# Kernel optimization log

Measured on AMD Instinct MI355X. Metric: run time of the kernel, lower is better.

## Reference

```python
import math
import jax, jax.numpy as jnp
import numpy as np

NUM_HEADS = 16
HIDDEN = 1024
FILL = -10000000000000.0


def setup_inputs() -> dict:
    key = jax.random.key(0)
    ks = jax.random.split(key, 12)
    B, S, H = 4, 2048, HIDDEN
    scale = 1.0 / math.sqrt(H)
    inp = {
        "query": jax.random.normal(ks[0], (B, S, H), jnp.float32),
        "key": jax.random.normal(ks[1], (B, S, H), jnp.float32),
        "value": jax.random.normal(ks[2], (B, S, H), jnp.float32),
        "mask": jnp.ones((B, S), jnp.float32),
        # torch.nn.Linear weights are [out, in]; y = x @ W.T + b
        "Wq": jax.random.normal(ks[3], (H, H), jnp.float32) * scale,
        "bq": jax.random.normal(ks[4], (H,), jnp.float32) * 0.01,
        "Wk": jax.random.normal(ks[5], (H, H), jnp.float32) * scale,
        "bk": jax.random.normal(ks[6], (H,), jnp.float32) * 0.01,
        "Wv": jax.random.normal(ks[7], (H, H), jnp.float32) * scale,
        "bv": jax.random.normal(ks[8], (H,), jnp.float32) * 0.01,
        "Wo": jax.random.normal(ks[9], (H, H), jnp.float32) * scale,
        "bo": jax.random.normal(ks[10], (H,), jnp.float32) * 0.01,
    }
    return inp


def reference(query, key, value, mask, Wq, bq, Wk, bk, Wv, bv, Wo, bo):
    B, S, H = query.shape
    nh = NUM_HEADS
    dh = H // nh

    def proj(x, W, b):
        # [B,S,H] -> [B,nh,S,dh]
        y = x @ W.T + b
        return y.reshape(B, S, nh, dh).transpose(0, 2, 1, 3)

    q = proj(query, Wq, bq)
    k = proj(key, Wk, bk)
    v = proj(value, Wv, bv)

    # mask_tril=True: combined padding + causal mask [B,1,S,S]
    tril = jnp.tril(jnp.ones((S, S), query.dtype))
    m = jnp.einsum("bs,ls->bls", mask, tril)[:, None]

    scores = jnp.einsum("bhqd,bhkd->bhqk", q, k) / math.sqrt(dh)
    scores = jnp.where(m == 0, jnp.asarray(FILL, scores.dtype), scores)
    probs = jax.nn.softmax(scores, axis=-1)  # dropout p=0 -> identity

    out = jnp.einsum("bhqv,bhvd->bhqd", probs, v)
    out = out.transpose(0, 2, 1, 3).reshape(B, S, H)
    return out @ Wo.T + bo
```

## Files before the change

kernel.cpp:

```cpp
#include <hip/hip_runtime.h>
#include <hip/hip_bf16.h>
#include <math.h>

#define BATCH 4
#define SEQ   2048
#define HID   1024
#define NH    16
#define DH    64
#define MTOT  (BATCH * SEQ)
#define FILLV (-1e13f)

typedef unsigned short ushort_t;
typedef short bf16x8 __attribute__((ext_vector_type(8)));
typedef float f32x4  __attribute__((ext_vector_type(4)));

__device__ __forceinline__ float bf2f(ushort_t u) {
    return __uint_as_float(((unsigned int)u) << 16);
}
__device__ __forceinline__ ushort_t f2bf(float f) {
    union { __hip_bfloat16 h; ushort_t u; } cv;
    cv.h = __float2bfloat16(f);
    return cv.u;
}

__device__ __forceinline__ void gload16(const void* g, void* l) {
    __builtin_amdgcn_global_load_lds(
        (const __attribute__((address_space(1))) unsigned int*)g,
        (__attribute__((address_space(3))) unsigned int*)l, 16, 0, 0);
}

__global__ __launch_bounds__(256) void cast_f32_bf16(
    const float* __restrict__ x, ushort_t* __restrict__ y, int n4)
{
    const int i = blockIdx.x * 256 + threadIdx.x;
    if (i < n4) {
        const float4 v = ((const float4*)x)[i];
        ushort4 o;
        o.x = f2bf(v.x); o.y = f2bf(v.y); o.z = f2bf(v.z); o.w = f2bf(v.w);
        ((ushort4*)y)[i] = o;
    }
}

template <bool OUT_BF16, bool BIAS_ROW>
__global__ __launch_bounds__(256) void gemm_bt_mfma(
    const ushort_t* __restrict__ A,
    const ushort_t* __restrict__ W,
    const float*    __restrict__ bias,
    void* __restrict__ Yv,
    int M, int N, int K)
{
    __shared__ ushort_t As[8 * 512];
    __shared__ ushort_t Bs[8 * 512];

    const int tid  = threadIdx.x;
    const int lane = tid & 63;
    const int wave = tid >> 6;
    const int wm   = wave & 1;
    const int wn   = wave >> 1;
    const int m0   = blockIdx.y * 128;
    const int n0   = blockIdx.x * 128;
    const int lr   = lane & 15;
    const int lk   = (lane >> 4) * 8;

    const ushort_t* aP = A + (size_t)(m0 + wave * 32 + lr) * K + lk;
    const ushort_t* wP = W + (size_t)(n0 + wave * 32 + lr) * K + lk;
    ushort_t* aL = &As[wave * 1024];
    ushort_t* bL = &Bs[wave * 1024];

    f32x4 acc[4][4];
#pragma unroll
    for (int i = 0; i < 4; i++)
#pragma unroll
        for (int j = 0; j < 4; j++) acc[i][j] = (f32x4){0.f, 0.f, 0.f, 0.f};

    for (int k0 = 0; k0 < K; k0 += 32) {
        gload16(aP,          aL);
        gload16(aP + 16 * K, aL + 512);
        gload16(wP,          bL);
        gload16(wP + 16 * K, bL + 512);
        aP += 32; wP += 32;
        __syncthreads();

        bf16x8 af[4], bf[4];
#pragma unroll
        for (int i = 0; i < 4; i++)
            af[i] = *(const bf16x8*)&As[(wm * 4 + i) * 512 + lane * 8];
#pragma unroll
        for (int j = 0; j < 4; j++)
            bf[j] = *(const bf16x8*)&Bs[(wn * 4 + j) * 512 + lane * 8];
#pragma unroll
        for (int i = 0; i < 4; i++)
#pragma unroll
            for (int j = 0; j < 4; j++)
                acc[i][j] = __builtin_amdgcn_mfma_f32_16x16x32_bf16(
                    af[i], bf[j], acc[i][j], 0, 0, 0);
        __syncthreads();
    }

    const int orow = (lane >> 4) * 4;
    const int ocol = lane & 15;

#pragma unroll
    for (int i = 0; i < 4; i++) {
#pragma unroll
        for (int j = 0; j < 4; j++) {
            const int col = n0 + wn * 64 + j * 16 + ocol;
#pragma unroll
            for (int r = 0; r < 4; r++) {
                const int row = m0 + wm * 64 + i * 16 + orow + r;
                const float bvv = BIAS_ROW ? bias[row] : bias[col];
                const float v = acc[i][j][r] + bvv;
                if (OUT_BF16)
                    ((ushort_t*)Yv)[(size_t)row * N + col] = f2bf(v);
                else
                    ((float*)Yv)[(size_t)row * N + col] = v;
            }
        }
    }
}

__global__ __launch_bounds__(256, 2) void attn_mfma(
    const ushort_t* __restrict__ Qp,
    const ushort_t* __restrict__ Kp,
    const ushort_t* __restrict__ Vt,
    const float*    __restrict__ mask,
    ushort_t* __restrict__ Op)
{
    __shared__ ushort_t Kl[2][4096];
    __shared__ ushort_t Vl[2][4096];
    __shared__ ushort_t PlA[4][16 * 72];
    __shared__ ushort_t PlB[4][16 * 72];

    const int tid  = threadIdx.x;
    const int lane = tid & 63;
    const int wave = tid >> 6;
    const int li   = lane & 15;
    const int lq   = lane >> 4;
    const int blk  = blockIdx.x;
    const int xcd = blk & 7;
    const int jj  = blk >> 3;
    const int bh  = xcd * 8 + (jj & 7);
    const int pp  = jj >> 3;
    const int pr  = pp * 4 + wave;
    const int h   = bh & (NH - 1);
    const int b   = bh >> 4;
    const int prow = lq * 4;

    const int q0a = pr * 16;
    const int q0b = (127 - pr) * 16;
    const int qrowA = q0a + li;
    const int qrowB = q0b + li;
    const int jmaxB = 31 - pp;

    const size_t bSEQ = (size_t)b * SEQ;
    const int    hoff = h * DH;

    const int srow = tid >> 3;
    const int scs8 = ((tid & 7) ^ (srow & 7)) * 8;

    const int fr0 = li * 64 + ((lq ^ (li & 7)) * 8);

    ushort_t* pwA = &PlA[wave][0];
    ushort_t* pwB = &PlB[wave][0];

    const float* mbase = mask + bSEQ + prow;

    const size_t qaA = (bSEQ + qrowA) * HID + hoff + lq * 8;
    const size_t qaB = (bSEQ + qrowB) * HID + hoff + lq * 8;
    const bf16x8 qfA0 = *(const bf16x8*)&Qp[qaA];
    const bf16x8 qfA1 = *(const bf16x8*)&Qp[qaA + 32];
    const bf16x8 qfB0 = *(const bf16x8*)&Qp[qaB];
    const bf16x8 qfB1 = *(const bf16x8*)&Qp[qaB + 32];

    f32x4 oaA[4], oaB[4];
#pragma unroll
    for (int nt = 0; nt < 4; nt++) {
        oaA[nt] = (f32x4){0.f, 0.f, 0.f, 0.f};
        oaB[nt] = (f32x4){0.f, 0.f, 0.f, 0.f};
    }
    float mA = -1e30f, lA = 0.f, mB = -1e30f, lB = 0.f;

    auto STAGE = [&](int js, int bs) {
        const size_t k0s = (size_t)js * 64;
        const ushort_t* kg = Kp + (bSEQ + k0s + srow) * HID + hoff + scs8;
        ushort_t* kl = &Kl[bs][wave * 512];
        gload16(kg, kl);
        gload16(kg + (size_t)32 * HID, kl + 2048);
        const ushort_t* vg = Vt + (size_t)(hoff + srow) * MTOT + bSEQ + k0s + scs8;
        ushort_t* vl = &Vl[bs][wave * 512];
        gload16(vg, vl);
        gload16(vg + (size_t)32 * MTOT, vl + 2048);
    };

    STAGE(0, 0);

    for (int j = 0; j <= jmaxB; ++j) {
        const int  k0  = j * 64;
        const int  bs  = j & 1;
        const bool doA = (j <= pp);

        f32x4 mk[4];
#pragma unroll
        for (int nt = 0; nt < 4; nt++)
            mk[nt] = *(const f32x4*)&mbase[k0 + nt * 16];
        __builtin_amdgcn_sched_barrier(0);

        const int jn = (j < jmaxB) ? (j + 1) : jmaxB;
        STAGE(jn, bs ^ 1);

        asm volatile("s_waitcnt vmcnt(8)" ::: "memory");
        __builtin_amdgcn_s_barrier();
        __builtin_amdgcn_sched_barrier(0);

        bf16x8 kf[4][2];
#pragma unroll
        for (int nt = 0; nt < 4; nt++) {
            const int eo = nt * 1024 + fr0;
            kf[nt][0] = *(const bf16x8*)&Kl[bs][eo];
            kf[nt][1] = *(const bf16x8*)&Kl[bs][eo ^ 32];
        }

        f32x4 saA[4], saB[4];
        __builtin_amdgcn_s_setprio(1);
#pragma unroll
        for (int nt = 0; nt < 4; nt++) {
            f32x4 a = (f32x4){0.f, 0.f, 0.f, 0.f};
            a = __builtin_amdgcn_mfma_f32_16x16x32_bf16(kf[nt][0], qfB0, a, 0, 0, 0);
            a = __builtin_amdgcn_mfma_f32_16x16x32_bf16(kf[nt][1], qfB1, a, 0, 0, 0);
            saB[nt] = a;
        }
        if (doA) {
#pragma unroll
            for (int nt = 0; nt < 4; nt++) {
                f32x4 a = (f32x4){0.f, 0.f, 0.f, 0.f};
                a = __builtin_amdgcn_mfma_f32_16x16x32_bf16(kf[nt][0], qfA0, a, 0, 0, 0);
                a = __builtin_amdgcn_mfma_f32_16x16x32_bf16(kf[nt][1], qfA1, a, 0, 0, 0);
                saA[nt] = a;
            }
        }
        __builtin_amdgcn_s_setprio(0);

        float sB[4][4];
#pragma unroll
        for (int nt = 0; nt < 4; nt++)
#pragma unroll
            for (int r = 0; r < 4; r++) {
                const float v = saB[nt][r] * 0.125f;
                sB[nt][r] = (mk[nt][r] == 0.f) ? FILLV : v;
            }
        if (k0 + 63 > q0b) {
#pragma unroll
            for (int nt = 0; nt < 4; nt++)
#pragma unroll
                for (int r = 0; r < 4; r++) {
                    const int kpos = k0 + nt * 16 + prow + r;
                    sB[nt][r] = (kpos > qrowB) ? FILLV : sB[nt][r];
                }
        }
        float pmB = fmaxf(fmaxf(sB[0][0], sB[0][1]), fmaxf(sB[0][2], sB[0][3]));
#pragma unroll
        for (int nt = 1; nt < 4; nt++)
            pmB = fmaxf(pmB, fmaxf(fmaxf(sB[nt][0], sB[nt][1]),
                                   fmaxf(sB[nt][2], sB[nt][3])));
        pmB = fmaxf(pmB, __shfl_xor(pmB, 16));
        pmB = fmaxf(pmB, __shfl_xor(pmB, 32));
        const float mnB = fmaxf(mB, pmB);
        const float alB = __expf(mB - mnB);
        mB = mnB;
        float psB = 0.f;
#pragma unroll
        for (int nt = 0; nt < 4; nt++) {
            const float p0 = __expf(sB[nt][0] - mnB);
            const float p1 = __expf(sB[nt][1] - mnB);
            const float p2 = __expf(sB[nt][2] - mnB);
            const float p3 = __expf(sB[nt][3] - mnB);
            psB += (p0 + p1) + (p2 + p3);
            ushort4 pk;
            pk.x = f2bf(p0); pk.y = f2bf(p1); pk.z = f2bf(p2); pk.w = f2bf(p3);
            *(ushort4*)&pwB[li * 72 + nt * 16 + prow] = pk;
        }
        psB += __shfl_xor(psB, 16);
        psB += __shfl_xor(psB, 32);
        lB = lB * alB + psB;

        float alA = 1.f;
        if (doA) {
            float sA[4][4];
#pragma unroll
            for (int nt = 0; nt < 4; nt++)
#pragma unroll
                for (int r = 0; r < 4; r++) {
                    const float v = saA[nt][r] * 0.125f;
                    sA[nt][r] = (mk[nt][r] == 0.f) ? FILLV : v;
                }
            if (k0 + 63 > q0a) {
#pragma unroll
                for (int nt = 0; nt < 4; nt++)
#pragma unroll
                    for (int r = 0; r < 4; r++) {
                        const int kpos = k0 + nt * 16 + prow + r;
                        sA[nt][r] = (kpos > qrowA) ? FILLV : sA[nt][r];
                    }
            }
            float pmA = fmaxf(fmaxf(sA[0][0], sA[0][1]), fmaxf(sA[0][2], sA[0][3]));
#pragma unroll
            for (int nt = 1; nt < 4; nt++)
                pmA = fmaxf(pmA, fmaxf(fmaxf(sA[nt][0], sA[nt][1]),
                                       fmaxf(sA[nt][2], sA[nt][3])));
            pmA = fmaxf(pmA, __shfl_xor(pmA, 16));
            pmA = fmaxf(pmA, __shfl_xor(pmA, 32));
            const float mnA = fmaxf(mA, pmA);
            alA = __expf(mA - mnA);
            mA = mnA;
            float psA = 0.f;
#pragma unroll
            for (int nt = 0; nt < 4; nt++) {
                const float p0 = __expf(sA[nt][0] - mnA);
                const float p1 = __expf(sA[nt][1] - mnA);
                const float p2 = __expf(sA[nt][2] - mnA);
                const float p3 = __expf(sA[nt][3] - mnA);
                psA += (p0 + p1) + (p2 + p3);
                ushort4 pk;
                pk.x = f2bf(p0); pk.y = f2bf(p1); pk.z = f2bf(p2); pk.w = f2bf(p3);
                *(ushort4*)&pwA[li * 72 + nt * 16 + prow] = pk;
            }
            psA += __shfl_xor(psA, 16);
            psA += __shfl_xor(psA, 32);
            lA = lA * alA + psA;
        }

        const bf16x8 pfB0 = *(const bf16x8*)&pwB[li * 72 + lq * 8];
        const bf16x8 pfB1 = *(const bf16x8*)&pwB[li * 72 + 32 + lq * 8];
        bf16x8 vf[4][2];
#pragma unroll
        for (int nt = 0; nt < 4; nt++) {
            const int eo = nt * 1024 + fr0;
            vf[nt][0] = *(const bf16x8*)&Vl[bs][eo];
            vf[nt][1] = *(const bf16x8*)&Vl[bs][eo ^ 32];
        }

        __builtin_amdgcn_s_setprio(1);
#pragma unroll
        for (int nt = 0; nt < 4; nt++) {
            f32x4 o = oaB[nt];
#pragma unroll
            for (int r = 0; r < 4; r++) o[r] *= alB;
            o = __builtin_amdgcn_mfma_f32_16x16x32_bf16(vf[nt][0], pfB0, o, 0, 0, 0);
            o = __builtin_amdgcn_mfma_f32_16x16x32_bf16(vf[nt][1], pfB1, o, 0, 0, 0);
            oaB[nt] = o;
        }
        __builtin_amdgcn_s_setprio(0);
        if (doA) {
            const bf16x8 pfA0 = *(const bf16x8*)&pwA[li * 72 + lq * 8];
            const bf16x8 pfA1 = *(const bf16x8*)&pwA[li * 72 + 32 + lq * 8];
            __builtin_amdgcn_s_setprio(1);
#pragma unroll
            for (int nt = 0; nt < 4; nt++) {
                f32x4 o = oaA[nt];
#pragma unroll
                for (int r = 0; r < 4; r++) o[r] *= alA;
                o = __builtin_amdgcn_mfma_f32_16x16x32_bf16(vf[nt][0], pfA0, o, 0, 0, 0);
                o = __builtin_amdgcn_mfma_f32_16x16x32_bf16(vf[nt][1], pfA1, o, 0, 0, 0);
                oaA[nt] = o;
            }
            __builtin_amdgcn_s_setprio(0);
        }

        __builtin_amdgcn_sched_barrier(0);
        __builtin_amdgcn_s_barrier();
    }
    asm volatile("s_waitcnt vmcnt(0)" ::: "memory");

    {
        const float linv = 1.f / lB;
        const size_t obase = (bSEQ + qrowB) * HID + hoff + prow;
#pragma unroll
        for (int nt = 0; nt < 4; nt++) {
            ushort4 ov;
            ov.x = f2bf(oaB[nt][0] * linv);
            ov.y = f2bf(oaB[nt][1] * linv);
            ov.z = f2bf(oaB[nt][2] * linv);
            ov.w = f2bf(oaB[nt][3] * linv);
            *(ushort4*)&Op[obase + nt * 16] = ov;
        }
    }
    {
        const float linv = 1.f / lA;
        const size_t obase = (bSEQ + qrowA) * HID + hoff + prow;
#pragma unroll
        for (int nt = 0; nt < 4; nt++) {
            ushort4 ov;
            ov.x = f2bf(oaA[nt][0] * linv);
            ov.y = f2bf(oaA[nt][1] * linv);
            ov.z = f2bf(oaA[nt][2] * linv);
            ov.w = f2bf(oaA[nt][3] * linv);
            *(ushort4*)&Op[obase + nt * 16] = ov;
        }
    }
}

extern "C" void kernel_launch(void* const* d_in, const int* in_sizes, int n_in,
                              void* d_out, int out_size, void* d_ws, size_t ws_size,
                              hipStream_t stream) {
    const float* query = (const float*)d_in[0];
    const float* key   = (const float*)d_in[1];
    const float* value = (const float*)d_in[2];
    const float* mask  = (const float*)d_in[3];
    const float* Wq    = (const float*)d_in[4];
    const float* bq    = (const float*)d_in[5];
    const float* Wk    = (const float*)d_in[6];
    const float* bk    = (const float*)d_in[7];
    const float* Wv    = (const float*)d_in[8];
    const float* bv    = (const float*)d_in[9];
    const float* Wo    = (const float*)d_in[10];
    const float* bo    = (const float*)d_in[11];

    const size_t eA = (size_t)MTOT * HID;
    const size_t eW = (size_t)HID * HID;
    ushort_t* qb  = (ushort_t*)d_ws;
    ushort_t* kb  = qb  + eA;
    ushort_t* vb  = kb  + eA;
    ushort_t* Qp  = vb  + eA;
    ushort_t* Kp  = Qp  + eA;
    ushort_t* Vtb = Kp  + eA;
    ushort_t* Op  = Vtb + eA;
    ushort_t* wqb = Op  + eA;
    ushort_t* wkb = wqb + eW;
    ushort_t* wvb = wkb + eW;
    ushort_t* wob = wvb + eW;

    const int n4a = (int)(eA / 4), n4w = (int)(eW / 4);
    cast_f32_bf16<<<(n4a + 255) / 256, 256, 0, stream>>>(query, qb, n4a);
    cast_f32_bf16<<<(n4a + 255) / 256, 256, 0, stream>>>(key,   kb, n4a);
    cast_f32_bf16<<<(n4a + 255) / 256, 256, 0, stream>>>(value, vb, n4a);
    cast_f32_bf16<<<(n4w + 255) / 256, 256, 0, stream>>>(Wq, wqb, n4w);
    cast_f32_bf16<<<(n4w + 255) / 256, 256, 0, stream>>>(Wk, wkb, n4w);
    cast_f32_bf16<<<(n4w + 255) / 256, 256, 0, stream>>>(Wv, wvb, n4w);
    cast_f32_bf16<<<(n4w + 255) / 256, 256, 0, stream>>>(Wo, wob, n4w);

    dim3 gg(HID / 128, MTOT / 128);
    gemm_bt_mfma<true, false><<<gg, 256, 0, stream>>>(qb, wqb, bq, Qp, MTOT, HID, HID);
    gemm_bt_mfma<true, false><<<gg, 256, 0, stream>>>(kb, wkb, bk, Kp, MTOT, HID, HID);
    dim3 gv(MTOT / 128, HID / 128);
    gemm_bt_mfma<true, true><<<gv, 256, 0, stream>>>(wvb, vb, bv, Vtb, HID, MTOT, HID);

    attn_mfma<<<(BATCH * NH * 64) / 4, 256, 0, stream>>>(Qp, Kp, Vtb, mask, Op);

    gemm_bt_mfma<false, false><<<gg, 256, 0, stream>>>(Op, wob, bo, d_out, MTOT, HID, HID);
}
```

Before: 420.4 us.

## Double-buffer GEMM LDS tiles and swizzle block order across XCDs

Converts the projection GEMM's K loop to a two-stage LDS double buffer: the next tile's direct-to-LDS loads are issued before computing the current one, with explicit vmcnt waits and raw barriers in place of __syncthreads. It also remaps the block index so consecutive blocks are grouped per XCD (eight-way interleave), aiming at better L2 locality. This doubles LDS use, and the swizzle assumes the grid size is divisible by 8. The attention kernel is unchanged, so only the GEMM share of total time is affected.

Result: faster. 411.9 us (-2.0%).

```diff
diff --git a/kernel.cpp b/kernel.cpp
--- a/kernel.cpp
+++ b/kernel.cpp
@@ -49,52 +49,73 @@
     void* __restrict__ Yv,
     int M, int N, int K)
 {
-    __shared__ ushort_t As[8 * 512];
-    __shared__ ushort_t Bs[8 * 512];
+    __shared__ ushort_t As[2][4096];
+    __shared__ ushort_t Bs[2][4096];
 
     const int tid  = threadIdx.x;
     const int lane = tid & 63;
     const int wave = tid >> 6;
     const int wm   = wave & 1;
     const int wn   = wave >> 1;
-    const int m0   = blockIdx.y * 128;
-    const int n0   = blockIdx.x * 128;
+
+    const int flat = blockIdx.y * gridDim.x + blockIdx.x;
+    const int cpx  = (gridDim.x * gridDim.y) >> 3;
+    const int fl2  = (flat & 7) * cpx + (flat >> 3);
+    const int bx   = fl2 % gridDim.x;
+    const int by   = fl2 / gridDim.x;
+
+    const int m0   = by * 128;
+    const int n0   = bx * 128;
     const int lr   = lane & 15;
     const int lk   = (lane >> 4) * 8;
 
-    const ushort_t* aP = A + (size_t)(m0 + wave * 32 + lr) * K + lk;
-    const ushort_t* wP = W + (size_t)(n0 + wave * 32 + lr) * K + lk;
-    ushort_t* aL = &As[wave * 1024];
-    ushort_t* bL = &Bs[wave * 1024];
-
     f32x4 acc[4][4];
 #pragma unroll
     for (int i = 0; i < 4; i++)
 #pragma unroll
         for (int j = 0; j < 4; j++) acc[i][j] = (f32x4){0.f, 0.f, 0.f, 0.f};
 
-    for (int k0 = 0; k0 < K; k0 += 32) {
-        gload16(aP,          aL);
-        gload16(aP + 16 * K, aL + 512);
-        gload16(wP,          bL);
-        gload16(wP + 16 * K, bL + 512);
-        aP += 32; wP += 32;
-        __syncthreads();
+    auto STAGE = [&](int kk, int d) {
+        const ushort_t* a = A + (size_t)(m0 + wave * 32 + lr) * K + kk + lk;
+        const ushort_t* w = W + (size_t)(n0 + wave * 32 + lr) * K + kk + lk;
+        ushort_t* al = &As[d][wave * 1024];
+        ushort_t* bl = &Bs[d][wave * 1024];
+        gload16(a,                 al);
+        gload16(a + (size_t)16 * K, al + 512);
+        gload16(w,                 bl);
+        gload16(w + (size_t)16 * K, bl + 512);
+    };
+
+    const int nk = K >> 5;
+    STAGE(0, 0);
+
+    for (int kt = 0; kt < nk; ++kt) {
+        const int d = kt & 1;
+        if (kt + 1 < nk) {
+            STAGE((kt + 1) << 5, d ^ 1);
+            asm volatile("s_waitcnt vmcnt(4)" ::: "memory");
+        } else {
+            asm volatile("s_waitcnt vmcnt(0)" ::: "memory");
+        }
+        __builtin_amdgcn_s_barrier();
+        __builtin_amdgcn_sched_barrier(0);
 
         bf16x8 af[4], bf[4];
 #pragma unroll
         for (int i = 0; i < 4; i++)
-            af[i] = *(const bf16x8*)&As[(wm * 4 + i) * 512 + lane * 8];
+            af[i] = *(const bf16x8*)&As[d][(wm * 4 + i) * 512 + lane * 8];
 #pragma unroll
         for (int j = 0; j < 4; j++)
-            bf[j] = *(const bf16x8*)&Bs[(wn * 4 + j) * 512 + lane * 8];
+            bf[j] = *(const bf16x8*)&Bs[d][(wn * 4 + j) * 512 + lane * 8];
 #pragma unroll
         for (int i = 0; i < 4; i++)
 #pragma unroll
             for (int j = 0; j < 4; j++)
                 acc[i][j] = __builtin_amdgcn_mfma_f32_16x16x32_bf16(
                     af[i], bf[j], acc[i][j], 0, 0, 0);
-        __syncthreads();
+
+        __builtin_amdgcn_sched_barrier(0);
+        __builtin_amdgcn_s_barrier();
     }
 
     const int orow = (lane >> 4) * 4;
```
